# Kernel tuning notes

Measured on AMD Instinct MI355X. Metric: run time of the kernel, lower is better.

## Reference

```python
import jax, jax.numpy as jnp
import numpy as np

B, S, A, H, NH = 4, 4096, 512, 1024, 16
HD = H // NH  # 64


def setup_inputs() -> dict:
    key = jax.random.key(0)
    ks = jax.random.split(key, 12)
    s = 1.0 / np.sqrt(H)
    return {
        "hidden_states": jax.random.normal(ks[0], (B, S, H), jnp.float32),
        "audio_tokens": jax.random.normal(ks[1], (B, A, H), jnp.float32),
        "attention_mask": jax.random.randint(ks[2], (B, A), 0, 2, jnp.int32),
        "Wq": jax.random.normal(ks[3], (H, H), jnp.float32) * s,
        "bq": jnp.zeros((H,), jnp.float32),
        "Wk": jax.random.normal(ks[4], (H, H), jnp.float32) * s,
        "bk": jnp.zeros((H,), jnp.float32),
        "Wv": jax.random.normal(ks[5], (H, H), jnp.float32) * s,
        "bv": jnp.zeros((H,), jnp.float32),
        "Wo": jax.random.normal(ks[6], (H, H), jnp.float32) * s,
        "bo": jnp.zeros((H,), jnp.float32),
        "ln_gamma": jnp.ones((H,), jnp.float32),
        "ln_beta": jnp.zeros((H,), jnp.float32),
        "residual_scale": jnp.asarray(0.05, jnp.float32),
    }


def _san(x, big=10000.0):
    return jnp.nan_to_num(x, nan=0.0, posinf=big, neginf=-big)


def reference(hidden_states, audio_tokens, attention_mask, Wq, bq, Wk, bk, Wv, bv,
              Wo, bo, ln_gamma, ln_beta, residual_scale):
    hs = _san(hidden_states).astype(jnp.float32)
    at = _san(audio_tokens).astype(jnp.float32)

    def heads(x, W, b):  # [b, t, H] -> [b, t, nh, hd]
        return _san(x @ W.T + b).reshape(x.shape[0], x.shape[1], NH, HD)

    q = heads(hs, Wq, bq)            # [B,S,NH,HD]
    k = heads(at, Wk, bk)            # [B,A,NH,HD]
    v = heads(at, Wv, bv)            # [B,A,NH,HD]

    scale = max(np.sqrt(HD), 1e-8)
    scores = jnp.einsum("bsnd,band->bnsa", q, k) / scale  # [B,NH,S,A]
    scores = jnp.clip(_san(jnp.clip(scores, -50.0, 50.0), 50.0), -50.0, 50.0)

    attend = (attention_mask > 0)[:, None, None, :]       # [B,1,1,A]
    scores = jnp.where(attend, scores, -10000.0)
    scores = jnp.clip(scores, -50.0, 50.0)

    probs = jax.nn.softmax(scores, axis=-1)
    probs = _san(probs, 1.0)
    probs = probs / (jnp.sum(probs, axis=-1, keepdims=True) + 1e-8)

    ctx = jnp.einsum("bnsa,band->bsnd", probs, v).reshape(B, S, H)
    delta = _san(ctx @ Wo.T + bo)

    rs = jnp.clip(residual_scale, 0.0, 0.3)
    delta = rs * delta

    mu = jnp.mean(delta, axis=-1, keepdims=True)
    var = jnp.mean(jnp.square(delta - mu), axis=-1, keepdims=True)
    delta = (delta - mu) / jnp.sqrt(var + 1e-5) * ln_gamma + ln_beta
    return delta
```

## Files before the change

kernel.cpp:

```cpp
#include <hip/hip_runtime.h>
#include <hip/hip_bf16.h>
#include <cstdint>
#include <cstddef>

#define B_  4
#define S_  4096
#define A_  512
#define H_  1024
#define NH_ 16
#define HD_ 64

typedef __bf16 bf16;
typedef __bf16 bf16x8 __attribute__((ext_vector_type(8)));
typedef __bf16 bf16x4 __attribute__((ext_vector_type(4)));
typedef float  fx4    __attribute__((ext_vector_type(4)));

typedef __attribute__((address_space(3))) void LDS_v;
typedef const __attribute__((address_space(1))) void GLB_v;

__device__ __forceinline__ void gl_lds16(const void* g, void* l) {
    __builtin_amdgcn_global_load_lds((GLB_v*)g, (LDS_v*)l, 16, 0, 0);
}

__device__ __forceinline__ float sanf(float x) {
    if (x != x) return 0.f;
    if (fabsf(x) == __builtin_inff()) return x > 0.f ? 10000.f : -10000.f;
    return x;
}

__global__ __launch_bounds__(256) void cast_all(const float* __restrict__ hs,
                                                const float* __restrict__ at,
                                                const float* __restrict__ wq,
                                                const float* __restrict__ wk,
                                                const float* __restrict__ wv,
                                                const float* __restrict__ wo,
                                                bf16* __restrict__ dhs, bf16* __restrict__ dat,
                                                bf16* __restrict__ dwq, bf16* __restrict__ dwk,
                                                bf16* __restrict__ dwv, bf16* __restrict__ dwo) {
    int i = blockIdx.x * 256 + threadIdx.x;
    const float* s; bf16* d; int off;
    if (i < 4194304)      { s = hs; d = dhs; off = i; }
    else if (i < 4718592) { s = at; d = dat; off = i - 4194304; }
    else if (i < 4980736) { s = wq; d = dwq; off = i - 4718592; }
    else if (i < 5242880) { s = wk; d = dwk; off = i - 4980736; }
    else if (i < 5505024) { s = wv; d = dwv; off = i - 5242880; }
    else                  { s = wo; d = dwo; off = i - 5505024; }
    float4 v = ((const float4*)s)[off];
    bf16x4 o;
    o[0] = (bf16)sanf(v.x); o[1] = (bf16)sanf(v.y);
    o[2] = (bf16)sanf(v.z); o[3] = (bf16)sanf(v.w);
    *(bf16x4*)&d[(size_t)off * 4] = o;
}


#define GEMM_PRO()                                                                     \
    STG(0, 0, 0, 0); STG(1, 0, 0, 0); STG(0, 1, 0, 0); STG(1, 1, 0, 0);                \
    asm volatile("s_waitcnt vmcnt(4)" ::: "memory");                                   \
    __builtin_amdgcn_s_barrier();

#define GEMM_PH(ACC0_, ACCOFF_, KS_, BI_, STGM_, STGH_, KN_, SI_, DOVM_)               \
    {                                                                                  \
        if (ACC0_) {                                                                   \
            for (int j2 = 0; j2 < 4; j2++) bfr[j2] = DSRB(j2, KS_, BI_);               \
        }                                                                              \
        for (int i = 0; i < 4; i++) af[i] = DSRA(i + ACCOFF_, KS_, BI_);               \
        STG(STGM_, STGH_, KN_, SI_);                                                   \
        __builtin_amdgcn_s_barrier();                                                  \
        asm volatile("s_waitcnt lgkmcnt(0)" ::: "memory");                             \
        __builtin_amdgcn_s_setprio(1);                                                 \
        for (int i = 0; i < 4; i++)                                                    \
            for (int j2 = 0; j2 < 4; j2++)                                             \
                acc[i + ACCOFF_][j2] = __builtin_amdgcn_mfma_f32_16x16x32_bf16(        \
                    af[i], bfr[j2], acc[i + ACCOFF_][j2], 0, 0, 0);                    \
        __builtin_amdgcn_s_setprio(0);                                                 \
        if (DOVM_) { asm volatile("s_waitcnt vmcnt(4)" ::: "memory"); }                \
        __builtin_amdgcn_s_barrier();                                                  \
    }

#define GEMM_BODY()                                                                    \
    fx4 acc[8][4] = {};                                                                \
    GEMM_PRO();                                                                        \
    for (int kt = 0; kt < 15; ++kt) {                                                  \
        const int bi = kt & 1, si = bi ^ 1, kn = kt + 1;                               \
        bf16x8 af[4], bfr[4];                                                          \
        GEMM_PH(1, 0, 0, bi, 0, 0, kn, si, 0)                                 \
        GEMM_PH(0, 4, 0, bi, 1, 0, kn, si, 1)                      \
        GEMM_PH(1, 0, 1, bi, 0, 1, kn, si, 0)                                 \
        GEMM_PH(0, 4, 1, bi, 1, 1, kn, si, 1)                      \
    }                                                                                  \
    {                                         \
        const int bi = 1;                                                              \
        bf16x8 af[4], bfr[4];                                                          \
        for (int j2 = 0; j2 < 4; j2++) bfr[j2] = DSRB(j2, 0, bi);                      \
        for (int i = 0; i < 4; i++) af[i] = DSRA(i, 0, bi);                            \
        __builtin_amdgcn_s_setprio(1);                                                 \
        for (int i = 0; i < 4; i++)                                                    \
            for (int j2 = 0; j2 < 4; j2++)                                             \
                acc[i][j2] = __builtin_amdgcn_mfma_f32_16x16x32_bf16(af[i], bfr[j2], acc[i][j2], 0, 0, 0); \
        __builtin_amdgcn_s_setprio(0);                                                 \
        for (int i = 0; i < 4; i++) af[i] = DSRA(i + 4, 0, bi);                        \
        __builtin_amdgcn_s_setprio(1);                                                 \
        for (int i = 0; i < 4; i++)                                                    \
            for (int j2 = 0; j2 < 4; j2++)                                             \
                acc[i + 4][j2] = __builtin_amdgcn_mfma_f32_16x16x32_bf16(af[i], bfr[j2], acc[i + 4][j2], 0, 0, 0); \
        __builtin_amdgcn_s_setprio(0);                                                 \
        asm volatile("s_waitcnt vmcnt(0)" ::: "memory");                               \
        __builtin_amdgcn_s_barrier();                                                  \
        for (int j2 = 0; j2 < 4; j2++) bfr[j2] = DSRB(j2, 1, bi);                      \
        for (int i = 0; i < 4; i++) af[i] = DSRA(i, 1, bi);                            \
        __builtin_amdgcn_s_setprio(1);                                                 \
        for (int i = 0; i < 4; i++)                                                    \
            for (int j2 = 0; j2 < 4; j2++)                                             \
                acc[i][j2] = __builtin_amdgcn_mfma_f32_16x16x32_bf16(af[i], bfr[j2], acc[i][j2], 0, 0, 0); \
        __builtin_amdgcn_s_setprio(0);                                                 \
        for (int i = 0; i < 4; i++) af[i] = DSRA(i + 4, 1, bi);                        \
        __builtin_amdgcn_s_setprio(1);                                                 \
        for (int i = 0; i < 4; i++)                                                    \
            for (int j2 = 0; j2 < 4; j2++)                                             \
                acc[i + 4][j2] = __builtin_amdgcn_mfma_f32_16x16x32_bf16(af[i], bfr[j2], acc[i + 4][j2], 0, 0, 0); \
        __builtin_amdgcn_s_setprio(0);                                                 \
    }

#define GEMM_COMMON_DECLS()                                                            \
    const int tid  = threadIdx.x;                                                      \
    const int lane = tid & 63;                                                         \
    const int w8   = tid >> 6;                                                         \
    const int wm   = w8 >> 2, wn = w8 & 3;                                             \
    const int lr   = lane & 15, kq = lane >> 4;                                        \
    const int swz  = (((lr >> 1) & 1) << 4) | (((lr >> 2) & 1) << 3);                  \
    const int g = lane ^ (((lane >> 3) & 1) << 1) ^ ((lane >> 4) & 1);

#define STG(MS_, kh_, kt_, si_) do {                                                   \
        const bf16* s_ = (MS_ ? Bsrc : Asrc) + (kt_) * 64 + (kh_) * 32;                \
        gl_lds16(s_,                 &lds[si_][MS_][kh_][w8 * 32][0]      + lane * 8); \
        gl_lds16(s_ + (size_t)16384, &lds[si_][MS_][kh_][w8 * 32 + 16][0] + lane * 8); \
    } while (0)

#define DSRA(i_, ks_, bi_) (*(const bf16x8*)(&lds[bi_][0][ks_][0][0] + \
        ((((wm * 128 + (i_) * 16 + lr) * 32 + kq * 8)) ^ swz)))
#define DSRB(j_, ks_, bi_) (*(const bf16x8*)(&lds[bi_][1][ks_][0][0] + \
        ((((wn * 64 + (j_) * 16 + lr) * 32 + kq * 8)) ^ swz)))

__global__ __launch_bounds__(512, 2) void gemm256qkv(const bf16* __restrict__ hsb,
                                                     const bf16* __restrict__ atb,
                                                     const bf16* __restrict__ wqb,
                                                     const bf16* __restrict__ wkb,
                                                     const bf16* __restrict__ wvb,
                                                     const float* __restrict__ bq,
                                                     const float* __restrict__ bk,
                                                     const float* __restrict__ bv,
                                                     bf16* __restrict__ Qb,
                                                     bf16* __restrict__ Kb,
                                                     bf16* __restrict__ Vtb) {
    __shared__ __align__(16) bf16 lds[2][2][2][256][32];

    GEMM_COMMON_DECLS();

    const int id = blockIdx.x;
    int mode, m0, n0;
    const bf16 *Ap, *Btp; const float* bias;
    if (id < 256) {
        const int xcd = id & 7, jj = id >> 3;
        mode = 0; m0 = (xcd * 8 + (jj >> 2)) << 8; n0 = (jj & 3) << 8;
        Ap = hsb; Btp = wqb; bias = bq;
    } else {
        int t = id - 256;
        mode = 1 + (t >> 5); t &= 31;
        m0 = (t >> 2) << 8; n0 = (t & 3) << 8;
        Ap = atb; Btp = (mode == 1) ? wkb : wvb; bias = (mode == 1) ? bk : bv;
    }

    const bf16* Asrc = Ap  + (size_t)(m0 + w8 * 32 + (g >> 2)) * 1024 + (g & 3) * 8;
    const bf16* Bsrc = Btp + (size_t)(n0 + w8 * 32 + (g >> 2)) * 1024 + (g & 3) * 8;

    GEMM_BODY();

    float bb[4];
#pragma unroll
    for (int j2 = 0; j2 < 4; j2++) bb[j2] = bias[n0 + wn * 64 + j2 * 16 + lr];

    if (mode == 0) {
        const float sc = 0.18033688011112042f;
#pragma unroll
        for (int i = 0; i < 8; i++) {
            int row = m0 + wm * 128 + i * 16 + kq * 4;
#pragma unroll
            for (int j2 = 0; j2 < 4; j2++) {
                int col = n0 + wn * 64 + j2 * 16 + lr;
#pragma unroll
                for (int r = 0; r < 4; r++)
                    Qb[(size_t)(row + r) * 1024 + col] = (bf16)((acc[i][j2][r] + bb[j2]) * sc);
            }
        }
    } else if (mode == 1) {
#pragma unroll
        for (int i = 0; i < 8; i++) {
            int row = m0 + wm * 128 + i * 16 + kq * 4;
#pragma unroll
            for (int j2 = 0; j2 < 4; j2++) {
                int col = n0 + wn * 64 + j2 * 16 + lr;
#pragma unroll
                for (int r = 0; r < 4; r++)
                    Kb[(size_t)(row + r) * 1024 + col] = (bf16)(acc[i][j2][r] + bb[j2]);
            }
        }
    } else {
#pragma unroll
        for (int i = 0; i < 8; i++) {
            int m = m0 + wm * 128 + i * 16 + kq * 4;
            int bidx = m >> 9, a = m & 511;
#pragma unroll
            for (int j2 = 0; j2 < 4; j2++) {
                int col = n0 + wn * 64 + j2 * 16 + lr;
                bf16x4 o;
#pragma unroll
                for (int r = 0; r < 4; r++) o[r] = (bf16)(acc[i][j2][r] + bb[j2]);
                *(bf16x4*)&Vtb[((size_t)bidx * H_ + col) * A_ + a] = o;
            }
        }
    }
}

__global__ __launch_bounds__(512, 2) void gemm256o(const bf16* __restrict__ A,
                                                   const bf16* __restrict__ Bt,
                                                   const float* __restrict__ bias,
                                                   bf16* __restrict__ C,
                                                   const float* __restrict__ rsp) {
    __shared__ __align__(16) bf16 lds[2][2][2][256][32];

    GEMM_COMMON_DECLS();

    const int xcd = blockIdx.x & 7, jj = blockIdx.x >> 3;
    const int m0 = (xcd * 8 + (jj >> 2)) << 8;
    const int n0 = (jj & 3) << 8;

    const bf16* Asrc = A  + (size_t)(m0 + w8 * 32 + (g >> 2)) * 1024 + (g & 3) * 8;
    const bf16* Bsrc = Bt + (size_t)(n0 + w8 * 32 + (g >> 2)) * 1024 + (g & 3) * 8;

    GEMM_BODY();

    float bb[4];
#pragma unroll
    for (int j2 = 0; j2 < 4; j2++) bb[j2] = bias[n0 + wn * 64 + j2 * 16 + lr];
    const float sc = fminf(fmaxf(rsp[0], 0.f), 0.3f);
#pragma unroll
    for (int i = 0; i < 8; i++) {
        int row = m0 + wm * 128 + i * 16 + kq * 4;
#pragma unroll
        for (int j2 = 0; j2 < 4; j2++) {
            int col = n0 + wn * 64 + j2 * 16 + lr;
#pragma unroll
            for (int r = 0; r < 4; r++)
                C[(size_t)(row + r) * 1024 + col] = (bf16)((acc[i][j2][r] + bb[j2]) * sc);
        }
    }
}

#undef STG
#undef DSRA
#undef DSRB
#undef GEMM_BODY
#undef GEMM_PH
#undef GEMM_PRO
#undef GEMM_COMMON_DECLS

__global__ __launch_bounds__(256, 4) void attn_kernel(const bf16* __restrict__ Q,
                                                      const bf16* __restrict__ Kb,
                                                      const bf16* __restrict__ Vt,
                                                      const int* __restrict__ mask,
                                                      bf16* __restrict__ ctx) {
    __shared__ __align__(16) bf16 Qs[128 * 72];
    __shared__ __align__(16) bf16 Ks[64 * 72];
    __shared__ __align__(16) bf16 Vts[64 * 72];
    __shared__ float smask[512];

    const int tid  = threadIdx.x;
    const int lane = tid & 63;
    const int wv   = tid >> 6;
    const int lr   = lane & 15, kq = lane >> 4;
    const int bid = blockIdx.x;
    const int h  = (bid & 7) | (((bid >> 3) & 1) << 3);
    const int b  = (bid >> 4) & 3;
    const int st = bid >> 6;
    const int m0 = b * S_ + st * 128;
    const float LO = -72.134752f;

    smask[tid]       = (mask[b * A_ + tid] > 0)       ? -LO : LO;
    smask[tid + 256] = (mask[b * A_ + tid + 256] > 0) ? -LO : LO;

    bf16x8 qreg[2][2];
#pragma unroll
    for (int kk2 = 0; kk2 < 2; kk2++)
#pragma unroll
        for (int nt = 0; nt < 2; nt++)
            qreg[kk2][nt] = *(const bf16x8*)(Q + (size_t)(m0 + wv * 32 + nt * 16 + lr) * H_
                                              + h * 64 + kk2 * 32 + kq * 8);

    const int srow = tid >> 2, sseg = tid & 3;
    const size_t kg = (size_t)(b * A_ + srow) * H_ + h * 64 + sseg * 16;
    const bf16* vrow = Vt + (size_t)(b * H_ + h * 64 + srow) * A_;
    const int va0 = 32 * (sseg >> 1) + 4 * ((2 * sseg) & 3);
    const int va1 = 32 * (sseg >> 1) + 4 * ((2 * sseg + 1) & 3);

    bf16x8 kr0 = *(const bf16x8*)(Kb + kg);
    bf16x8 kr1 = *(const bf16x8*)(Kb + kg + 8);
    bf16x4 v00 = *(const bf16x4*)(vrow + va0);
    bf16x4 v01 = *(const bf16x4*)(vrow + va0 + 16);
    bf16x4 v10 = *(const bf16x4*)(vrow + va1);
    bf16x4 v11 = *(const bf16x4*)(vrow + va1 + 16);

    fx4 acco[2][4] = {};
    fx4 accd[2] = {};

    bf16x8 vone;
#pragma unroll
    for (int e = 0; e < 8; e++) vone[e] = (bf16)1.0f;

    for (int it = 0; it < 8; it++) {
        const int a0 = it * 64;
        __syncthreads();
        *(bf16x8*)&Ks[srow * 72 + sseg * 16]      = kr0;
        *(bf16x8*)&Ks[srow * 72 + sseg * 16 + 8]  = kr1;
        *(bf16x8*)&Vts[srow * 72 + sseg * 16] =
            __builtin_shufflevector(v00, v01, 0, 1, 2, 3, 4, 5, 6, 7);
        *(bf16x8*)&Vts[srow * 72 + sseg * 16 + 8] =
            __builtin_shufflevector(v10, v11, 0, 1, 2, 3, 4, 5, 6, 7);
        __syncthreads();

        if (it < 7) {
            const size_t ko = kg + (size_t)(a0 + 64) * H_;
            kr0 = *(const bf16x8*)(Kb + ko);
            kr1 = *(const bf16x8*)(Kb + ko + 8);
            v00 = *(const bf16x4*)(vrow + a0 + 64 + va0);
            v01 = *(const bf16x4*)(vrow + a0 + 64 + va0 + 16);
            v10 = *(const bf16x4*)(vrow + a0 + 64 + va1);
            v11 = *(const bf16x4*)(vrow + a0 + 64 + va1 + 16);
        }

        fx4 accs[4][2] = {};
#pragma unroll
        for (int kk2 = 0; kk2 < 2; kk2++) {
            bf16x8 kf[4];
#pragma unroll
            for (int mt = 0; mt < 4; mt++)
                kf[mt] = *(const bf16x8*)&Ks[(mt * 16 + lr) * 72 + kk2 * 32 + kq * 8];
#pragma unroll
            for (int mt = 0; mt < 4; mt++)
#pragma unroll
                for (int nt = 0; nt < 2; nt++)
                    accs[mt][nt] = __builtin_amdgcn_mfma_f32_16x16x32_bf16(kf[mt], qreg[kk2][nt], accs[mt][nt], 0, 0, 0);
        }

        bf16x8 pa[2][2];
#pragma unroll
        for (int mt = 0; mt < 4; mt++) {
            fx4 cap = *(const fx4*)&smask[a0 + mt * 16 + kq * 4];
#pragma unroll
            for (int nt = 0; nt < 2; nt++) {
#pragma unroll
                for (int r = 0; r < 4; r++) {
                    float p = __builtin_amdgcn_exp2f(fminf(accs[mt][nt][r], cap[r]));
                    pa[mt >> 1][nt][(mt & 1) * 4 + r] = (bf16)p;
                }
            }
        }

#pragma unroll
        for (int ks = 0; ks < 2; ks++) {
#pragma unroll
            for (int stl = 0; stl < 2; stl++)
                accd[stl] = __builtin_amdgcn_mfma_f32_16x16x32_bf16(pa[ks][stl], vone, accd[stl], 0, 0, 0);
#pragma unroll
            for (int dt = 0; dt < 4; dt++) {
                bf16x8 vf = *(const bf16x8*)&Vts[(dt * 16 + lr) * 72 + ks * 32 + kq * 8];
#pragma unroll
                for (int stl = 0; stl < 2; stl++)
                    acco[stl][dt] = __builtin_amdgcn_mfma_f32_16x16x32_bf16(pa[ks][stl], vf, acco[stl][dt], 0, 0, 0);
            }
        }
    }

#pragma unroll
    for (int stl = 0; stl < 2; stl++) {
        float ri[4];
#pragma unroll
        for (int r = 0; r < 4; r++) ri[r] = __builtin_amdgcn_rcpf(accd[stl][r]);
#pragma unroll
        for (int dt = 0; dt < 4; dt++)
#pragma unroll
            for (int r = 0; r < 4; r++)
                Qs[(wv * 32 + stl * 16 + kq * 4 + r) * 72 + dt * 16 + lr] =
                    (bf16)(acco[stl][dt][r] * ri[r]);
    }
    __syncthreads();
#pragma unroll
    for (int i = 0; i < 4; i++) {
        int c = tid + i * 256, row = c >> 3, ch = c & 7;
        *(bf16x8*)&ctx[(size_t)(m0 + row) * H_ + h * 64 + ch * 8] = *(const bf16x8*)&Qs[row * 72 + ch * 8];
    }
}

__global__ __launch_bounds__(256) void ln_kernel(const bf16* __restrict__ in,
                                                 float* __restrict__ out,
                                                 const float* __restrict__ gamma,
                                                 const float* __restrict__ beta) {
    __shared__ float red[8];
    const int tid = threadIdx.x;
    const int row = ((blockIdx.x & 7) << 11) | (blockIdx.x >> 3);
    bf16x4 xb = *(const bf16x4*)&in[(size_t)row * 1024 + tid * 4];
    float x0 = (float)xb[0], x1 = (float)xb[1], x2 = (float)xb[2], x3 = (float)xb[3];
    float s = x0 + x1 + x2 + x3;
    float q = x0 * x0 + x1 * x1 + x2 * x2 + x3 * x3;
#pragma unroll
    for (int off = 32; off > 0; off >>= 1) {
        s += __shfl_down(s, off);
        q += __shfl_down(q, off);
    }
    if ((tid & 63) == 0) { red[(tid >> 6) * 2] = s; red[(tid >> 6) * 2 + 1] = q; }
    __syncthreads();
    s = red[0] + red[2] + red[4] + red[6];
    q = red[1] + red[3] + red[5] + red[7];
    float mean = s * (1.f / 1024.f);
    float var  = q * (1.f / 1024.f) - mean * mean;
    float inv  = rsqrtf(var + 1e-5f);
    float4 g  = ((const float4*)gamma)[tid];
    float4 bb = ((const float4*)beta)[tid];
    float4 y;
    y.x = (x0 - mean) * inv * g.x + bb.x;
    y.y = (x1 - mean) * inv * g.y + bb.y;
    y.z = (x2 - mean) * inv * g.z + bb.z;
    y.w = (x3 - mean) * inv * g.w + bb.w;
    ((float4*)(out + (size_t)row * 1024))[tid] = y;
}

extern "C" void kernel_launch(void* const* d_in, const int* in_sizes, int n_in,
                              void* d_out, int out_size, void* d_ws, size_t ws_size,
                              hipStream_t stream) {
    const float* hs    = (const float*)d_in[0];
    const float* at    = (const float*)d_in[1];
    const int*   maskp = (const int*)d_in[2];
    const float* Wq    = (const float*)d_in[3];
    const float* bq    = (const float*)d_in[4];
    const float* Wk    = (const float*)d_in[5];
    const float* bk    = (const float*)d_in[6];
    const float* Wv    = (const float*)d_in[7];
    const float* bv    = (const float*)d_in[8];
    const float* Wo    = (const float*)d_in[9];
    const float* bo    = (const float*)d_in[10];
    const float* gamma = (const float*)d_in[11];
    const float* beta  = (const float*)d_in[12];
    const float* rsp   = (const float*)d_in[13];

    char* ws = (char*)d_ws;
    bf16* hsb = (bf16*)(ws + 0);
    bf16* ctx = (bf16*)(ws + 0);
    bf16* atb = (bf16*)(ws + 33554432);
    bf16* wqb = (bf16*)(ws + 37748736);
    bf16* wkb = (bf16*)(ws + 39845888);
    bf16* wvb = (bf16*)(ws + 41943040);
    bf16* wob = (bf16*)(ws + 44040192);
    bf16* Qb  = (bf16*)(ws + 46137344);
    bf16* Ob  = Qb;
    bf16* Kb  = (bf16*)(ws + 79691776);
    bf16* Vtb = (bf16*)(ws + 83886080);

    cast_all<<<22528, 256, 0, stream>>>(hs, at, Wq, Wk, Wv, Wo,
                                        hsb, atb, wqb, wkb, wvb, wob);

    gemm256qkv<<<320, 512, 0, stream>>>(hsb, atb, wqb, wkb, wvb,
                                        bq, bk, bv, Qb, Kb, Vtb);

    attn_kernel<<<2048, 256, 0, stream>>>(Qb, Kb, Vtb, maskp, ctx);

    gemm256o<<<256, 512, 0, stream>>>(ctx, wob, bo, Ob, rsp);
    ln_kernel<<<16384, 256, 0, stream>>>(Ob, (float*)d_out, gamma, beta);
}
```

Before: 319.9 us.

## Split fused QKV GEMM into a separate small-tile K/V GEMM and Q GEMM

The fused QKV launch had 320 blocks of 256x256 tiles, so on a 256-CU device it ran as one full wave plus a 64-block tail. The K/V projection now runs in its own kernel with 128x128 tiles (256 blocks) and a simple single-buffered loop. The Q projection keeps the tuned 256x256 kernel with exactly 256 blocks. This trades the tail for an extra launch and a less optimized, unpipelined K/V GEMM.

```diff
diff --git a/kernel.cpp b/kernel.cpp
--- a/kernel.cpp
+++ b/kernel.cpp
@@ -141,82 +141,36 @@
 #define DSRB(j_, ks_, bi_) (*(const bf16x8*)(&lds[bi_][1][ks_][0][0] + \
         ((((wn * 64 + (j_) * 16 + lr) * 32 + kq * 8)) ^ swz)))
 
-__global__ __launch_bounds__(512, 2) void gemm256qkv(const bf16* __restrict__ hsb,
-                                                     const bf16* __restrict__ atb,
-                                                     const bf16* __restrict__ wqb,
-                                                     const bf16* __restrict__ wkb,
-                                                     const bf16* __restrict__ wvb,
-                                                     const float* __restrict__ bq,
-                                                     const float* __restrict__ bk,
-                                                     const float* __restrict__ bv,
-                                                     bf16* __restrict__ Qb,
-                                                     bf16* __restrict__ Kb,
-                                                     bf16* __restrict__ Vtb) {
+__global__ __launch_bounds__(512, 2) void gemm256q(const bf16* __restrict__ hsb,
+                                                   const bf16* __restrict__ wqb,
+                                                   const float* __restrict__ bq,
+                                                   bf16* __restrict__ Qb) {
     __shared__ __align__(16) bf16 lds[2][2][2][256][32];
 
     GEMM_COMMON_DECLS();
 
-    const int id = blockIdx.x;
-    int mode, m0, n0;
-    const bf16 *Ap, *Btp; const float* bias;
-    if (id < 256) {
-        const int xcd = id & 7, jj = id >> 3;
-        mode = 0; m0 = (xcd * 8 + (jj >> 2)) << 8; n0 = (jj & 3) << 8;
-        Ap = hsb; Btp = wqb; bias = bq;
-    } else {
-        int t = id - 256;
-        mode = 1 + (t >> 5); t &= 31;
-        m0 = (t >> 2) << 8; n0 = (t & 3) << 8;
-        Ap = atb; Btp = (mode == 1) ? wkb : wvb; bias = (mode == 1) ? bk : bv;
-    }
-
-    const bf16* Asrc = Ap  + (size_t)(m0 + w8 * 32 + (g >> 2)) * 1024 + (g & 3) * 8;
-    const bf16* Bsrc = Btp + (size_t)(n0 + w8 * 32 + (g >> 2)) * 1024 + (g & 3) * 8;
+    const int xcd = blockIdx.x & 7, jj = blockIdx.x >> 3;
+    const int m0 = (xcd * 8 + (jj >> 2)) << 8;
+    const int n0 = (jj & 3) << 8;
+
+    const bf16* Asrc = hsb + (size_t)(m0 + w8 * 32 + (g >> 2)) * 1024 + (g & 3) * 8;
+    const bf16* Bsrc = wqb + (size_t)(n0 + w8 * 32 + (g >> 2)) * 1024 + (g & 3) * 8;
 
     GEMM_BODY();
 
     float bb[4];
 #pragma unroll
-    for (int j2 = 0; j2 < 4; j2++) bb[j2] = bias[n0 + wn * 64 + j2 * 16 + lr];
-
-    if (mode == 0) {
-        const float sc = 0.18033688011112042f;
-#pragma unroll
-        for (int i = 0; i < 8; i++) {
-            int row = m0 + wm * 128 + i * 16 + kq * 4;
-#pragma unroll
-            for (int j2 = 0; j2 < 4; j2++) {
-                int col = n0 + wn * 64 + j2 * 16 + lr;
-#pragma unroll
-                for (int r = 0; r < 4; r++)
-                    Qb[(size_t)(row + r) * 1024 + col] = (bf16)((acc[i][j2][r] + bb[j2]) * sc);
-            }
-        }
-    } else if (mode == 1) {
-#pragma unroll
-        for (int i = 0; i < 8; i++) {
-            int row = m0 + wm * 128 + i * 16 + kq * 4;
-#pragma unroll
-            for (int j2 = 0; j2 < 4; j2++) {
-                int col = n0 + wn * 64 + j2 * 16 + lr;
-#pragma unroll
-                for (int r = 0; r < 4; r++)
-                    Kb[(size_t)(row + r) * 1024 + col] = (bf16)(acc[i][j2][r] + bb[j2]);
-            }
-        }
-    } else {
-#pragma unroll
-        for (int i = 0; i < 8; i++) {
-            int m = m0 + wm * 128 + i * 16 + kq * 4;
-            int bidx = m >> 9, a = m & 511;
-#pragma unroll
-            for (int j2 = 0; j2 < 4; j2++) {
-                int col = n0 + wn * 64 + j2 * 16 + lr;
-                bf16x4 o;
-#pragma unroll
-                for (int r = 0; r < 4; r++) o[r] = (bf16)(acc[i][j2][r] + bb[j2]);
-                *(bf16x4*)&Vtb[((size_t)bidx * H_ + col) * A_ + a] = o;
-            }
+    for (int j2 = 0; j2 < 4; j2++) bb[j2] = bq[n0 + wn * 64 + j2 * 16 + lr];
+    const float sc = 0.18033688011112042f;
+#pragma unroll
+    for (int i = 0; i < 8; i++) {
+        int row = m0 + wm * 128 + i * 16 + kq * 4;
+#pragma unroll
+        for (int j2 = 0; j2 < 4; j2++) {
+            int col = n0 + wn * 64 + j2 * 16 + lr;
+#pragma unroll
+            for (int r = 0; r < 4; r++)
+                Qb[(size_t)(row + r) * 1024 + col] = (bf16)((acc[i][j2][r] + bb[j2]) * sc);
         }
     }
 }
@@ -263,6 +217,88 @@
 #undef GEMM_PH
 #undef GEMM_PRO
 #undef GEMM_COMMON_DECLS
+
+__global__ __launch_bounds__(256) void kv_gemm(const bf16* __restrict__ atb,
+                                               const bf16* __restrict__ wkb,
+                                               const bf16* __restrict__ wvb,
+                                               const float* __restrict__ bk,
+                                               const float* __restrict__ bv,
+                                               bf16* __restrict__ Kb,
+                                               bf16* __restrict__ Vtb) {
+    __shared__ __align__(16) bf16 As[128 * 32];
+    __shared__ __align__(16) bf16 Bs[128 * 32];
+
+    const int id = blockIdx.x;
+    int mode, m0, n0;
+    const bf16 *Bt; const float* bias;
+    if (id < 128) { mode = 1; m0 = (id & 15) * 128; n0 = (id >> 4) * 128; Bt = wkb; bias = bk; }
+    else          { int t = id - 128; mode = 2; m0 = (t & 15) * 128; n0 = (t >> 4) * 128; Bt = wvb; bias = bv; }
+
+    const int tid  = threadIdx.x;
+    const int lane = tid & 63;
+    const int wv   = tid >> 6;
+    const int wr   = wv >> 1, wc = wv & 1;
+    const int lr   = lane & 15, kq = lane >> 4;
+
+    fx4 acc[4][4] = {};
+
+    const bf16* Ag = atb + (size_t)m0 * 1024;
+    const bf16* Bg = Bt  + (size_t)n0 * 1024;
+    const int c0 = tid, c1 = tid + 256;
+    const int row0 = c0 >> 2, kc0 = c0 & 3;
+    const int row1 = c1 >> 2, kc1 = c1 & 3;
+
+    for (int k0 = 0; k0 < 1024; k0 += 32) {
+        gl_lds16(Ag + (size_t)row0 * 1024 + k0 + kc0 * 8, &As[c0 * 8]);
+        gl_lds16(Ag + (size_t)row1 * 1024 + k0 + kc1 * 8, &As[c1 * 8]);
+        gl_lds16(Bg + (size_t)row0 * 1024 + k0 + kc0 * 8, &Bs[c0 * 8]);
+        gl_lds16(Bg + (size_t)row1 * 1024 + k0 + kc1 * 8, &Bs[c1 * 8]);
+        __syncthreads();
+        bf16x8 af[4], bfr[4];
+#pragma unroll
+        for (int i = 0; i < 4; i++) af[i]  = *(const bf16x8*)&As[(wr * 64 + i * 16 + lr) * 32 + kq * 8];
+#pragma unroll
+        for (int j = 0; j < 4; j++) bfr[j] = *(const bf16x8*)&Bs[(wc * 64 + j * 16 + lr) * 32 + kq * 8];
+#pragma unroll
+        for (int i = 0; i < 4; i++)
+#pragma unroll
+            for (int j = 0; j < 4; j++)
+                acc[i][j] = __builtin_amdgcn_mfma_f32_16x16x32_bf16(af[i], bfr[j], acc[i][j], 0, 0, 0);
+        __syncthreads();
+    }
+
+    float bb[4];
+#pragma unroll
+    for (int j = 0; j < 4; j++) bb[j] = bias[n0 + wc * 64 + j * 16 + lr];
+
+    if (mode == 1) {
+#pragma unroll
+        for (int i = 0; i < 4; i++) {
+            int row = m0 + wr * 64 + i * 16 + kq * 4;
+#pragma unroll
+            for (int j = 0; j < 4; j++) {
+                int col = n0 + wc * 64 + j * 16 + lr;
+#pragma unroll
+                for (int r = 0; r < 4; r++)
+                    Kb[(size_t)(row + r) * 1024 + col] = (bf16)(acc[i][j][r] + bb[j]);
+            }
+        }
+    } else {
+#pragma unroll
+        for (int i = 0; i < 4; i++) {
+            int m = m0 + wr * 64 + i * 16 + kq * 4;
+            int bidx = m >> 9, a = m & 511;
+#pragma unroll
+            for (int j = 0; j < 4; j++) {
+                int col = n0 + wc * 64 + j * 16 + lr;
+                bf16x4 o;
+#pragma unroll
+                for (int r = 0; r < 4; r++) o[r] = (bf16)(acc[i][j][r] + bb[j]);
+                *(bf16x4*)&Vtb[((size_t)bidx * H_ + col) * A_ + a] = o;
+            }
+        }
+    }
+}
 
 __global__ __launch_bounds__(256, 4) void attn_kernel(const bf16* __restrict__ Q,
                                                       const bf16* __restrict__ Kb,
@@ -467,8 +503,9 @@
     cast_all<<<22528, 256, 0, stream>>>(hs, at, Wq, Wk, Wv, Wo,
                                         hsb, atb, wqb, wkb, wvb, wob);
 
-    gemm256qkv<<<320, 512, 0, stream>>>(hsb, atb, wqb, wkb, wvb,
-                                        bq, bk, bv, Qb, Kb, Vtb);
+    kv_gemm<<<256, 256, 0, stream>>>(atb, wkb, wvb, bk, bv, Kb, Vtb);
+
+    gemm256q<<<256, 512, 0, stream>>>(hsb, wqb, bq, Qb);
 
     attn_kernel<<<2048, 256, 0, stream>>>(Qb, Kb, Vtb, maskp, ctx);
 
```

Result: faster. 308.2 us (-3.7%).
